# Optimization experiments

Measured on AMD Instinct MI355X. Metric: run time of the kernel, lower is better.

Reference implementation:

```python
import jax, jax.numpy as jnp
import numpy as np
from jax import lax

K = 3      # kernel_size
C = 64     # n_feat
B, H, W = 2, 256, 256


def _conv(x, w, b, pad):
    # NCHW conv, stride 1
    out = lax.conv_general_dilated(x, w, (1, 1), [(pad, pad), (pad, pad)],
                                   dimension_numbers=('NCHW', 'OIHW', 'NCHW'))
    return out + b[None, :, None, None]


def _prelu(x, a):
    # nn.PReLU() with a single shared learnable slope (init 0.25)
    return jnp.where(x >= 0, x, a * x)


def setup_inputs():
    key = jax.random.key(0)
    ks = jax.random.split(key, 20)
    s = 0.05
    def w(k, shape):
        return jax.random.normal(k, shape, jnp.float32) * s
    inp = {
        'image': jax.random.normal(ks[0], (B, C, H, W), jnp.float32),
        'guidance': jax.random.normal(ks[1], (B, C, H, W), jnp.float32),
        # self.tensor: 1x1 conv (2C -> C) + PReLU (shared with jbf_conv's act)
        'tensor_w': w(ks[2], (C, 2 * C, 1, 1)),
        'tensor_b': jnp.zeros((C,), jnp.float32),
        'a_jbf': jnp.full((1,), 0.25, jnp.float32),
        'kg_w1': w(ks[3], (C, C, 3, 3)), 'kg_b1': jnp.zeros((C,), jnp.float32),
        'kg_w2': w(ks[4], (C, C, 3, 3)), 'kg_b2': jnp.zeros((C,), jnp.float32),
        'kg_w3': w(ks[5], (C, C, 3, 3)), 'kg_b3': jnp.zeros((C,), jnp.float32),
        'kg_w4': w(ks[6], (C, C, 3, 3)), 'kg_b4': jnp.zeros((C,), jnp.float32),
        'kg_w5': w(ks[7], (K * K * C, C, 1, 1)),
        'kg_b5': jnp.zeros((K * K * C,), jnp.float32),
        'a_kg': jnp.full((1,), 0.25, jnp.float32),
        # jbf_conv: 3x3 C->C, PReLU (shared a_jbf), 3x3 C->C
        'jbf_w1': w(ks[8], (C, C, 3, 3)), 'jbf_b1': jnp.zeros((C,), jnp.float32),
        'jbf_w2': w(ks[9], (C, C, 3, 3)), 'jbf_b2': jnp.zeros((C,), jnp.float32),
    }
    return inp


def reference(image, guidance, tensor_w, tensor_b, a_jbf,
              kg_w1, kg_b1, kg_w2, kg_b2, kg_w3, kg_b3, kg_w4, kg_b4,
              kg_w5, kg_b5, a_kg, jbf_w1, jbf_b1, jbf_w2, jbf_b2):
    b, c, h, w = image.shape
    # fuse target+guidance features
    t = _prelu(_conv(jnp.concatenate([image, guidance], axis=1), tensor_w, tensor_b, 0), a_jbf)
    # concat_kg: predict per-pixel dynamic kernel (b, K*K*c, h, w)
    y = t
    for wt, bs in ((kg_w1, kg_b1), (kg_w2, kg_b2), (kg_w3, kg_b3), (kg_w4, kg_b4)):
        y = _prelu(_conv(y, wt, bs, 1), a_kg)
    bi_kernel = _conv(y, kg_w5, kg_b5, 0)
    # unfold: torch layout is channel-major (c, ki, kj) along dim 1
    p = (K - 1) // 2
    xp = jnp.pad(image, ((0, 0), (0, 0), (p, p), (p, p)))
    taps = [xp[:, :, i:i + h, j:j + w] for i in range(K) for j in range(K)]
    patch = jnp.stack(taps, axis=2).reshape(b, c * K * K, h, w)
    # NOTE: faithful to source -- (c*K*K) flat layout reinterpreted as (K*K, c)
    jbf = (patch * bi_kernel).reshape(b, K * K, c, h, w).sum(axis=1)
    out = _conv(_prelu(_conv(jbf, jbf_w1, jbf_b1, 1), a_jbf), jbf_w2, jbf_b2, 1)
    return out + image
```

## Files before the change

### kernel.cpp

```cpp
#include <hip/hip_runtime.h>

#define HW 65536

typedef __bf16 bf16x8 __attribute__((ext_vector_type(8)));
typedef float f32x16 __attribute__((ext_vector_type(16)));

__device__ inline unsigned short f2bf(float x) {
    union { float f; unsigned u; } v; v.f = x;
    unsigned r = v.u + 0x7FFF + ((v.u >> 16) & 1);
    return (unsigned short)(r >> 16);
}
__device__ inline float bfhi2f(unsigned u) {
    union { unsigned u; float f; } v; v.u = u & 0xffff0000u; return v.f;
}
__device__ inline float bflo2f(unsigned u) {
    union { unsigned u; float f; } v; v.u = u << 16; return v.f;
}

union FragU { uint4 u; bf16x8 v; };
__device__ inline bf16x8 ld_frag(const uint4* p) { FragU t; t.u = *p; return t.v; }

__global__ __launch_bounds__(256) void k_wprep(
    const float* __restrict__ w0, const float* __restrict__ w1,
    const float* __restrict__ w2, const float* __restrict__ w3,
    const float* __restrict__ w4, const float* __restrict__ w5,
    const float* __restrict__ w5c, const float* __restrict__ tw,
    unsigned short* __restrict__ wT)
{
    int y = blockIdx.y;
    unsigned short* o = wT + (size_t)y * 36864;
    if (y < 6) {
        const float* ws_[6] = {w0, w1, w2, w3, w4, w5};
        const float* w = ws_[y];
        for (int e = blockIdx.x * 256 + threadIdx.x; e < 36864; e += gridDim.x * 256) {
            int tap = e >> 12, oc = (e >> 6) & 63, ic = e & 63;
            int igg = ic >> 3, j = ic & 7;
            int dst = ((tap * 8 + igg) * 64 + oc) * 8 + j;
            o[dst] = f2bf(w[(oc * 64 + ic) * 9 + tap]);
        }
    } else if (y == 6) {
        for (int e = blockIdx.x * 256 + threadIdx.x; e < 36864; e += gridDim.x * 256)
            o[e] = f2bf(w5c[e]);
    } else {
        for (int e = blockIdx.x * 256 + threadIdx.x; e < 8192; e += gridDim.x * 256) {
            int oc = e >> 7, ic = e & 127;
            int kg = ic >> 3, j = ic & 7;
            o[((kg * 64 + oc) << 3) + j] = f2bf(tw[e]);
        }
    }
}

__global__ __launch_bounds__(256) void k_tr(
    const float* __restrict__ img, const float* __restrict__ gd,
    unsigned short* __restrict__ imgT, unsigned short* __restrict__ gdT)
{
    __shared__ float sT[64 * 66];
    int tid = threadIdx.x;
    int z = blockIdx.y;
    int b = z & 1;
    const float* src = (z >> 1) ? gd : img;
    unsigned short* dst = (z >> 1) ? gdT : imgT;
    int px0 = blockIdx.x * 64;
    size_t sbase = (size_t)b * 64 * HW + px0;

#pragma unroll
    for (int i = 0; i < 4; ++i) {
        int e = i * 256 + tid;
        int ic = e >> 4, seg = e & 15;
        float4 v = *(const float4*)(src + sbase + (size_t)ic * HW + seg * 4);
        float* p = &sT[ic * 66 + seg * 4];
        ((float2*)p)[0] = make_float2(v.x, v.y);
        ((float2*)p)[1] = make_float2(v.z, v.w);
    }
    __syncthreads();

    size_t dbase = (size_t)b * HW * 64 + (size_t)px0 * 64;
#pragma unroll
    for (int k = 0; k < 2; ++k) {
        int idx = k * 256 + tid;
        int px = idx >> 3, u = idx & 7;
        union { uint4 q; unsigned short h[8]; } o;
#pragma unroll
        for (int j = 0; j < 8; ++j)
            o.h[j] = f2bf(sT[(u * 8 + j) * 66 + px]);
        *(uint4*)(dst + dbase + (size_t)px * 64 + u * 8) = o.q;
    }
}

__global__ __launch_bounds__(256, 4) void k_fusem(
    const unsigned short* __restrict__ imgT, const unsigned short* __restrict__ gdT,
    const unsigned short* __restrict__ wTf, const float* __restrict__ bias,
    const float* __restrict__ a, unsigned short* __restrict__ out)
{
    __shared__ __align__(16) char smem[18688];
    uint4* sX = (uint4*)smem;
    float* sB = (float*)(smem + 18432);
    unsigned short* sT16 = (unsigned short*)smem;

    int tid = threadIdx.x;
    int wv = tid >> 6, lane = tid & 63;
    int half = lane >> 5, l31 = lane & 31;
    int b = blockIdx.z;
    int y0 = blockIdx.y * 8, x0 = blockIdx.x * 16;
    size_t zbase = (size_t)b * HW * 64;
    const uint4* wg = (const uint4*)wTf;

    if (tid < 64) sB[tid] = bias[tid];

    f32x16 acc[2];
#pragma unroll
    for (int i = 0; i < 2; ++i)
#pragma unroll
        for (int r = 0; r < 16; ++r) acc[i][r] = 0.f;

    auto loadX = [&](const unsigned short* src, uint4* rx) {
#pragma unroll
        for (int i = 0; i < 4; ++i) {
            int e = i * 256 + tid;
            int px = e >> 3, ig = e & 7;
            int gy = y0 + (px >> 4), gx = x0 + (px & 15);
            rx[i] = *(const uint4*)(src + zbase + ((size_t)(gy * 256 + gx)) * 64 + ig * 8);
        }
    };
    auto writeX = [&](const uint4* rx) {
#pragma unroll
        for (int i = 0; i < 4; ++i) {
            int e = i * 256 + tid;
            sX[(e >> 3) * 9 + (e & 7)] = rx[i];
        }
    };
    auto compute = [&](int h) {
#pragma unroll
        for (int c = 0; c < 4; ++c) {
            int ig = c * 2 + half;
            int kg = h * 8 + ig;
            bf16x8 a0 = ld_frag(&wg[kg * 64 + l31]);
            bf16x8 a1 = ld_frag(&wg[kg * 64 + 32 + l31]);
            int p0 = wv * 32 + l31;
            bf16x8 b0 = ld_frag(&sX[p0 * 9 + ig]);
            acc[0] = __builtin_amdgcn_mfma_f32_32x32x16_bf16(a0, b0, acc[0], 0, 0, 0);
            acc[1] = __builtin_amdgcn_mfma_f32_32x32x16_bf16(a1, b0, acc[1], 0, 0, 0);
        }
    };

    uint4 rx[4], ry[4];
    loadX(imgT, rx);
    writeX(rx);
    loadX(gdT, ry);
    __syncthreads();
    compute(0);
    __syncthreads();
    writeX(ry);
    __syncthreads();
    compute(1);

    float slope = a[0];
    __syncthreads();
    {
        int px = wv * 32 + l31;
#pragma unroll
        for (int ot = 0; ot < 2; ++ot)
#pragma unroll
            for (int q2 = 0; q2 < 4; ++q2) {
                unsigned short hw[4];
#pragma unroll
                for (int j = 0; j < 4; ++j) {
                    int r = (q2 << 2) | j;
                    int oc = ot * 32 + j + 8 * q2 + 4 * half;
                    float v = acc[ot][r] + sB[oc];
                    v = (v >= 0.f) ? v : slope * v;
                    hw[j] = f2bf(v);
                }
                int unit = ot * 4 + q2;
                int up = unit ^ (px & 7);
                uint2* p = (uint2*)&sT16[px * 64 + up * 8 + half * 4];
                *p = make_uint2((unsigned)hw[0] | ((unsigned)hw[1] << 16),
                                (unsigned)hw[2] | ((unsigned)hw[3] << 16));
            }
    }
    __syncthreads();
#pragma unroll
    for (int k = 0; k < 4; ++k) {
        int idx = k * 256 + tid;
        int row = idx >> 7, rem = idx & 127;
        int col = rem >> 3, u = rem & 7;
        int px = row * 16 + col;
        uint4 v = *(uint4*)&sT16[px * 64 + (u ^ (px & 7)) * 8];
        *(uint4*)(out + zbase + ((size_t)((y0 + row) * 256 + x0 + col)) * 64 + u * 8) = v;
    }
}

#define XU 5

template<int MODE>
__global__ __launch_bounds__(256, 4) void k_conv2x(
    const unsigned short* __restrict__ in,
    const unsigned short* __restrict__ w1T, const unsigned short* __restrict__ w2T,
    const float* __restrict__ b1, const float* __restrict__ b2,
    const float* __restrict__ a, const float* __restrict__ res,
    void* __restrict__ outv)
{
    __shared__ __align__(16) char smem[38912];
    uint4* sIn0 = (uint4*)smem;
    uint4* sIn1 = (uint4*)(smem + 19200);
    float* sB = (float*)(smem + 38400);

    int tid = threadIdx.x;
    int wv = tid >> 6, lane = tid & 63;
    int half = lane >> 5, l31 = lane & 31;
    int w2 = wv >> 1, g = wv & 1;
    int b = blockIdx.z;
    int y0 = blockIdx.y * 8, x0 = blockIdx.x * 16;
    const size_t zbase = (size_t)b * HW * 64;
    const uint4* wg1 = (const uint4*)w1T;
    const uint4* wg2 = (const uint4*)w2T;

    if (tid < 64) sB[tid] = b1[tid];
    else if (tid < 128) sB[tid] = b2[tid - 64];

    auto loadIn = [&](int h, uint4* rx) {
#pragma unroll
        for (int i = 0; i < 4; ++i) {
            int e = i * 256 + tid;
            int cell = e >> 2, ig = e & 3;
            int r = cell / 20, c2 = cell - r * 20;
            int gy = y0 - 2 + r, gx = x0 - 2 + c2;
            rx[i] = make_uint4(0, 0, 0, 0);
            bool act = (i < 3) || (e < 960);
            if (act && gy >= 0 && gy < 256 && gx >= 0 && gx < 256)
                rx[i] = *(const uint4*)(in + zbase + ((size_t)(gy * 256 + gx)) * 64 + h * 32 + ig * 8);
        }
    };
    auto writeIn = [&](uint4* s, const uint4* rx) {
#pragma unroll
        for (int i = 0; i < 4; ++i) {
            int e = i * 256 + tid;
            if (i < 3 || e < 960) s[(e >> 2) * XU + (e & 3)] = rx[i];
        }
    };

    int cellv[3], ibv[3];
#pragma unroll
    for (int s = 0; s < 3; ++s) {
        int c = g * 96 + s * 32 + l31;
        cellv[s] = c;
        int cc = c < 180 ? c : 179;
        ibv[s] = (cc / 18) * 20 + (cc % 18);
    }

    f32x16 acc1[3];
#pragma unroll
    for (int s = 0; s < 3; ++s)
#pragma unroll
        for (int r = 0; r < 16; ++r) acc1[s][r] = 0.f;

    auto conv1_h = [&](int h, const uint4* sInp) {
#pragma unroll
        for (int dy = 0; dy < 3; ++dy) {
#pragma unroll
            for (int dx = 0; dx < 3; ++dx) {
                int tap = dy * 3 + dx;
                int doff = dy * 20 + dx;
#pragma unroll
                for (int c = 0; c < 2; ++c) {
                    int ig = c * 2 + half;
                    bf16x8 af = ld_frag(&wg1[(tap * 8 + h * 4 + ig) * 64 + w2 * 32 + l31]);
#pragma unroll
                    for (int s = 0; s < 3; ++s) {
                        bf16x8 bb = ld_frag(&sInp[(ibv[s] + doff) * XU + ig]);
                        acc1[s] = __builtin_amdgcn_mfma_f32_32x32x16_bf16(af, bb, acc1[s], 0, 0, 0);
                    }
                }
            }
        }
    };

    uint4 rx[4];
    loadIn(0, rx);
    writeIn(sIn0, rx);
    uint4 ry[4];
    loadIn(1, ry);
    __syncthreads();
    conv1_h(0, sIn0);
    writeIn(sIn1, ry);
    __syncthreads();
    conv1_h(1, sIn1);

    float s1 = a[0];
    __syncthreads();
    unsigned short* sC16 = (unsigned short*)smem;
#pragma unroll
    for (int s = 0; s < 3; ++s) {
        int cell = cellv[s];
        if (cell < 180) {
            int orow = cell / 18, ocol = cell - orow * 18;
            int gy = y0 - 1 + orow, gx = x0 - 1 + ocol;
            bool inb = (gy >= 0 && gy < 256 && gx >= 0 && gx < 256);
#pragma unroll
            for (int q2 = 0; q2 < 4; ++q2) {
                unsigned short hw[4];
#pragma unroll
                for (int j = 0; j < 4; ++j) {
                    int r = (q2 << 2) | j;
                    int oc = w2 * 32 + j + 8 * q2 + 4 * half;
                    float v = acc1[s][r] + sB[oc];
                    v = (v >= 0.f) ? v : s1 * v;
                    if (!inb) v = 0.f;
                    hw[j] = f2bf(v);
                }
                int up = (w2 * 4 + q2) ^ (cell & 7);
                *(uint2*)&sC16[cell * 64 + up * 8 + half * 4] =
                    make_uint2((unsigned)hw[0] | ((unsigned)hw[1] << 16),
                               (unsigned)hw[2] | ((unsigned)hw[3] << 16));
            }
        }
    }
    __syncthreads();

    f32x16 acc2[2];
#pragma unroll
    for (int s = 0; s < 2; ++s)
#pragma unroll
        for (int r = 0; r < 16; ++r) acc2[s][r] = 0.f;

    int rowS[2], colS[2];
#pragma unroll
    for (int s = 0; s < 2; ++s) {
        int px = g * 64 + s * 32 + l31;
        rowS[s] = px >> 4; colS[s] = px & 15;
    }
    {
        const uint4* sC4 = (const uint4*)smem;
#pragma unroll
        for (int dy = 0; dy < 3; ++dy) {
#pragma unroll
            for (int dx = 0; dx < 3; ++dx) {
                int tap = dy * 3 + dx;
#pragma unroll
                for (int c = 0; c < 4; ++c) {
                    int ig = c * 2 + half;
                    bf16x8 af = ld_frag(&wg2[(tap * 8 + ig) * 64 + w2 * 32 + l31]);
#pragma unroll
                    for (int s = 0; s < 2; ++s) {
                        int cl = (rowS[s] + dy) * 18 + colS[s] + dx;
                        bf16x8 bb = ld_frag(&sC4[cl * 8 + (ig ^ (cl & 7))]);
                        acc2[s] = __builtin_amdgcn_mfma_f32_32x32x16_bf16(af, bb, acc2[s], 0, 0, 0);
                    }
                }
            }
        }
    }

    if (MODE == 0) {
        __syncthreads();
        unsigned short* sT16 = (unsigned short*)smem;
#pragma unroll
        for (int s = 0; s < 2; ++s) {
            int px = g * 64 + s * 32 + l31;
#pragma unroll
            for (int q2 = 0; q2 < 4; ++q2) {
                unsigned short hw[4];
#pragma unroll
                for (int j = 0; j < 4; ++j) {
                    int r = (q2 << 2) | j;
                    int oc = w2 * 32 + j + 8 * q2 + 4 * half;
                    float v = acc2[s][r] + sB[64 + oc];
                    v = (v >= 0.f) ? v : s1 * v;
                    hw[j] = f2bf(v);
                }
                int up = (w2 * 4 + q2) ^ (px & 7);
                uint2* p = (uint2*)&sT16[px * 64 + up * 8 + half * 4];
                *p = make_uint2((unsigned)hw[0] | ((unsigned)hw[1] << 16),
                                (unsigned)hw[2] | ((unsigned)hw[3] << 16));
            }
        }
        __syncthreads();
        unsigned short* outT = (unsigned short*)outv;
#pragma unroll
        for (int k = 0; k < 4; ++k) {
            int idx = k * 256 + tid;
            int row = idx >> 7, rem = idx & 127;
            int col = rem >> 3, u = rem & 7;
            int px = row * 16 + col;
            uint4 v = *(uint4*)&sT16[px * 64 + (u ^ (px & 7)) * 8];
            *(uint4*)(outT + zbase + ((size_t)((y0 + row) * 256 + x0 + col)) * 64 + u * 8) = v;
        }
    } else {
        float* outF = (float*)outv;
#pragma unroll
        for (int s = 0; s < 2; ++s) {
            int px = g * 64 + s * 32 + l31;
            int y = y0 + (px >> 4), x = x0 + (px & 15);
            size_t pbase = (size_t)b * 64 * HW + (size_t)y * 256 + x;
#pragma unroll
            for (int r = 0; r < 16; ++r) {
                int oc = w2 * 32 + (r & 3) + 8 * (r >> 2) + 4 * half;
                float v = acc2[s][r] + sB[64 + oc];
                v += res[pbase + (size_t)oc * HW];
                outF[pbase + (size_t)oc * HW] = v;
            }
        }
    }
}

struct OffTab { unsigned v[9][32]; int chlo[9]; };
constexpr OffTab make_tab() {
    OffTab t{};
    for (int kk = 0; kk < 9; ++kk) {
        int chlo = (kk * 64) / 9;
        t.chlo[kk] = chlo;
        for (int ot = 0; ot < 2; ++ot)
            for (int r = 0; r < 16; ++r) {
                int cc0 = ot * 32 + (r & 3) + 8 * (r >> 2);
                int q0 = kk * 64 + cc0, q1 = q0 + 4;
                int o0 = (q0 / 9 - chlo) * 360 + (q0 % 9 / 3) * 40 + (q0 % 9 % 3);
                int o1 = (q1 / 9 - chlo) * 360 + (q1 % 9 / 3) * 40 + (q1 % 9 % 3);
                t.v[kk][ot * 16 + r] = (unsigned)o0 | ((unsigned)o1 << 16);
            }
    }
    return t;
}
__constant__ OffTab kOff = make_tab();

__global__ __launch_bounds__(256, 2) void k_jbfm(
    const unsigned short* __restrict__ y4, const float* __restrict__ img,
    const unsigned short* __restrict__ w5T, const float* __restrict__ b5,
    unsigned short* __restrict__ out)
{
    __shared__ __align__(16) char smem[78592];
    uint4* sY = (uint4*)smem;
    float* sB5 = (float*)(smem + 76288);
    unsigned short* sT16 = (unsigned short*)smem;

    int tid = threadIdx.x;
    int wv = tid >> 6, lane = tid & 63;
    int half = lane >> 5, l31 = lane & 31;
    int b = blockIdx.z;
    int y0 = blockIdx.y * 8, x0 = blockIdx.x * 32;
    size_t zbase = (size_t)b * HW * 64;
    size_t ibase = (size_t)b * 64 * HW;

    int p_off[3], p_dst[3];
    bool p_a[3], p_b[3], p_act[3];
#pragma unroll
    for (int i = 0; i < 3; ++i) {
        int e = i * 256 + tid;
        bool act = e < 720;
        int ch = e / 90, rem = e - ch * 90;
        int rp = rem / 10, seg = rem - rp * 10;
        int gy = y0 + rp - 1;
        int gxb = x0 - 4 + seg * 4;
        bool xok = (gxb >= 0 && gxb < 256);
        p_act[i] = act;
        p_a[i] = act && xok && gy >= 0 && gy < 256;
        p_b[i] = act && xok && (gy + 1) < 256;
        p_off[i] = ch * HW + gy * 256 + gxb;
        p_dst[i] = ch * 360 + rp * 40 + seg * 4;
    }

#pragma unroll
    for (int i = 0; i < 8; ++i) {
        int e = i * 256 + tid;
        int px = e >> 3, ig = e & 7;
        int gy = y0 + (px >> 5), gx = x0 + (px & 31);
        sY[px * 9 + ig] = *(const uint4*)(y4 + zbase + ((size_t)(gy * 256 + gx)) * 64 + ig * 8);
    }
    for (int e = tid; e < 576; e += 256) sB5[e] = b5[e];

    {
        uint4* sW50 = (uint4*)(smem + 36864);
        unsigned* sP0 = (unsigned*)(smem + 53248);
#pragma unroll
        for (int u = 0; u < 2; ++u) {
            int uu = u * 256 + tid;
            int cc = uu & 63, ig = uu >> 6;
            sW50[uu] = ((const uint4*)w5T)[cc * 8 + ig];
        }
        const float* rp0 = img + ibase;
#pragma unroll
        for (int i = 0; i < 3; ++i) {
            float4 fa = make_float4(0, 0, 0, 0), fb = make_float4(0, 0, 0, 0);
            if (p_a[i]) fa = *(const float4*)(rp0 + p_off[i]);
            if (p_b[i]) fb = *(const float4*)(rp0 + p_off[i] + 256);
            if (p_act[i]) {
                uint4 pk;
                pk.x = (unsigned)f2bf(fa.x) | ((unsigned)f2bf(fb.x) << 16);
                pk.y = (unsigned)f2bf(fa.y) | ((unsigned)f2bf(fb.y) << 16);
                pk.z = (unsigned)f2bf(fa.z) | ((unsigned)f2bf(fb.z) << 16);
                pk.w = (unsigned)f2bf(fa.w) | ((unsigned)f2bf(fb.w) << 16);
                *(uint4*)&sP0[p_dst[i]] = pk;
            }
        }
    }

    float jb[2][2][16];
#pragma unroll
    for (int i = 0; i < 2; ++i)
#pragma unroll
        for (int j = 0; j < 2; ++j)
#pragma unroll
            for (int r = 0; r < 16; ++r) jb[i][j][r] = 0.f;

    __syncthreads();

#pragma unroll 1
    for (int kk = 0; kk < 9; ++kk) {
        const int cur = kk & 1;
        const uint4* sW5c = (const uint4*)(smem + 36864 + cur * 8192);
        const unsigned* sPc = (const unsigned*)(smem + 53248 + cur * 11520);

        uint4 wpre0, wpre1;
        float4 pfa[3], pfb[3];
        if (kk < 8) {
            const int nk = kk + 1;
            const int chlo_n = kOff.chlo[nk];
            {
                int cc = tid & 63, ig = tid >> 6;
                wpre0 = ((const uint4*)w5T)[(nk * 64 + cc) * 8 + ig];
                int uu = 256 + tid;
                int cc1 = uu & 63, ig1 = uu >> 6;
                wpre1 = ((const uint4*)w5T)[(nk * 64 + cc1) * 8 + ig1];
            }
            const float* rp0 = img + ibase + (size_t)chlo_n * HW;
#pragma unroll
            for (int i = 0; i < 3; ++i) {
                pfa[i] = make_float4(0, 0, 0, 0);
                pfb[i] = make_float4(0, 0, 0, 0);
                if (p_a[i]) pfa[i] = *(const float4*)(rp0 + p_off[i]);
                if (p_b[i]) pfb[i] = *(const float4*)(rp0 + p_off[i] + 256);
            }
        }

        f32x16 acc[2][2];
#pragma unroll
        for (int ot = 0; ot < 2; ++ot)
#pragma unroll
            for (int r = 0; r < 16; ++r) {
                int cc0 = ot * 32 + (r & 3) + 8 * (r >> 2);
                float bv = sB5[kk * 64 + cc0 + 4 * half];
                acc[ot][0][r] = bv;
                acc[ot][1][r] = bv;
            }

#pragma unroll
        for (int c = 0; c < 4; ++c) {
            int ig = c * 2 + half;
            bf16x8 a0 = ld_frag(&sW5c[ig * 64 + l31]);
            bf16x8 a1 = ld_frag(&sW5c[ig * 64 + 32 + l31]);
            int p0 = wv * 64 + l31;
            bf16x8 b0 = ld_frag(&sY[p0 * 9 + ig]);
            bf16x8 b1 = ld_frag(&sY[(p0 + 32) * 9 + ig]);
            acc[0][0] = __builtin_amdgcn_mfma_f32_32x32x16_bf16(a0, b0, acc[0][0], 0, 0, 0);
            acc[0][1] = __builtin_amdgcn_mfma_f32_32x32x16_bf16(a0, b1, acc[0][1], 0, 0, 0);
            acc[1][0] = __builtin_amdgcn_mfma_f32_32x32x16_bf16(a1, b0, acc[1][0], 0, 0, 0);
            acc[1][1] = __builtin_amdgcn_mfma_f32_32x32x16_bf16(a1, b1, acc[1][1], 0, 0, 0);
        }

        {
            const unsigned* basep = sPc + wv * 80 + l31 + 3;
            const unsigned* tab = kOff.v[kk];
#pragma unroll
            for (int ot = 0; ot < 2; ++ot)
#pragma unroll
                for (int r = 0; r < 16; ++r) {
                    unsigned oo = tab[ot * 16 + r];
                    unsigned o0 = oo & 0xffffu, o1 = oo >> 16;
                    unsigned pv = basep[half ? o1 : o0];
                    jb[ot][0][r] = fmaf(acc[ot][0][r], bflo2f(pv), jb[ot][0][r]);
                    jb[ot][1][r] = fmaf(acc[ot][1][r], bfhi2f(pv), jb[ot][1][r]);
                }
        }

        if (kk < 8) {
            uint4* sW5n = (uint4*)(smem + 36864 + (cur ^ 1) * 8192);
            unsigned* sPn = (unsigned*)(smem + 53248 + (cur ^ 1) * 11520);
            sW5n[tid] = wpre0;
            sW5n[256 + tid] = wpre1;
#pragma unroll
            for (int i = 0; i < 3; ++i) {
                if (p_act[i]) {
                    uint4 pk;
                    pk.x = (unsigned)f2bf(pfa[i].x) | ((unsigned)f2bf(pfb[i].x) << 16);
                    pk.y = (unsigned)f2bf(pfa[i].y) | ((unsigned)f2bf(pfb[i].y) << 16);
                    pk.z = (unsigned)f2bf(pfa[i].z) | ((unsigned)f2bf(pfb[i].z) << 16);
                    pk.w = (unsigned)f2bf(pfa[i].w) | ((unsigned)f2bf(pfb[i].w) << 16);
                    *(uint4*)&sPn[p_dst[i]] = pk;
                }
            }
        }
        __syncthreads();
    }

#pragma unroll
    for (int ot = 0; ot < 2; ++ot)
#pragma unroll
        for (int pt = 0; pt < 2; ++pt) {
            int px = wv * 64 + pt * 32 + l31;
#pragma unroll
            for (int q2 = 0; q2 < 4; ++q2) {
                unsigned short hw[4];
#pragma unroll
                for (int j = 0; j < 4; ++j) {
                    int r = (q2 << 2) | j;
                    hw[j] = f2bf(jb[ot][pt][r]);
                }
                int unit = ot * 4 + q2;
                int up = unit ^ (px & 7);
                uint2* p = (uint2*)&sT16[px * 64 + up * 8 + half * 4];
                *p = make_uint2((unsigned)hw[0] | ((unsigned)hw[1] << 16),
                                (unsigned)hw[2] | ((unsigned)hw[3] << 16));
            }
        }
    __syncthreads();
#pragma unroll
    for (int k = 0; k < 8; ++k) {
        int col = tid >> 3, u = tid & 7;
        int px = k * 32 + col;
        uint4 v = *(uint4*)&sT16[px * 64 + (u ^ (px & 7)) * 8];
        *(uint4*)(out + zbase + ((size_t)((y0 + k) * 256 + x0 + col)) * 64 + u * 8) = v;
    }
}

extern "C" void kernel_launch(void* const* d_in, const int* in_sizes, int n_in,
                              void* d_out, int out_size, void* d_ws, size_t ws_size,
                              hipStream_t stream) {
    const float* img  = (const float*)d_in[0];
    const float* gd   = (const float*)d_in[1];
    const float* tw   = (const float*)d_in[2];
    const float* tb   = (const float*)d_in[3];
    const float* ajbf = (const float*)d_in[4];
    const float* kw1  = (const float*)d_in[5];
    const float* kb1  = (const float*)d_in[6];
    const float* kw2  = (const float*)d_in[7];
    const float* kb2  = (const float*)d_in[8];
    const float* kw3  = (const float*)d_in[9];
    const float* kb3  = (const float*)d_in[10];
    const float* kw4  = (const float*)d_in[11];
    const float* kb4  = (const float*)d_in[12];
    const float* kw5  = (const float*)d_in[13];
    const float* kb5  = (const float*)d_in[14];
    const float* akg  = (const float*)d_in[15];
    const float* jw1  = (const float*)d_in[16];
    const float* jb1  = (const float*)d_in[17];
    const float* jw2  = (const float*)d_in[18];
    const float* jb2  = (const float*)d_in[19];
    float* out  = (float*)d_out;

    const size_t TEN = (size_t)2 * HW * 64;
    unsigned short* bufA = (unsigned short*)d_ws;
    unsigned short* imgT = bufA + TEN;
    unsigned short* gdT  = imgT + TEN;
    unsigned short* wT   = gdT + TEN;
    unsigned short* bufB = (unsigned short*)d_out;
    unsigned short* bufC = gdT;

    dim3 gs(16, 32, 2);
    dim3 gw(8, 32, 2);

    k_tr<<<dim3(1024, 4), 256, 0, stream>>>(img, gd, imgT, gdT);
    k_wprep<<<dim3(4, 8), 256, 0, stream>>>(kw1, kw2, kw3, kw4, jw1, jw2, kw5, tw, wT);

    k_fusem<<<gs, 256, 0, stream>>>(imgT, gdT, wT + (size_t)7 * 36864, tb, ajbf, bufA);

    k_conv2x<0><<<gs, 256, 0, stream>>>(bufA, wT + (size_t)0 * 36864, wT + (size_t)1 * 36864,
                                        kb1, kb2, akg, nullptr, bufB);
    k_conv2x<0><<<gs, 256, 0, stream>>>(bufB, wT + (size_t)2 * 36864, wT + (size_t)3 * 36864,
                                        kb3, kb4, akg, nullptr, bufA);

    k_jbfm<<<gw, 256, 0, stream>>>(bufA, img, wT + (size_t)6 * 36864, kb5, bufC);

    k_conv2x<2><<<gs, 256, 0, stream>>>(bufC, wT + (size_t)4 * 36864, wT + (size_t)5 * 36864,
                                        jb1, jb2, ajbf, img, out);
}
```

Baseline: 311.5 us.

## Fuse conv stages into one persistent cooperative kernel with grid barriers

Replaces the five separate stage launches (fuse, two double-conv, jbf, final double-conv) with one persistent 512-block kernel. The blocks loop over tiles and synchronise between stages with a software grid barrier built on an atomic counter that k_wprep resets. This removes launch gaps and per-kernel tail effects. In exchange, every block uses the largest shared-memory footprint (78 KB) at occupancy 2, so the conv stages lose occupancy, and each stage boundary adds barrier spin cost.

Result: slower. 762.6 us (+144.8%).

```diff
diff --git a/kernel.cpp b/kernel.cpp
--- a/kernel.cpp
+++ b/kernel.cpp
@@ -25,10 +25,11 @@
     const float* __restrict__ w2, const float* __restrict__ w3,
     const float* __restrict__ w4, const float* __restrict__ w5,
     const float* __restrict__ w5c, const float* __restrict__ tw,
-    unsigned short* __restrict__ wT)
+    unsigned short* __restrict__ wT, unsigned long long* __restrict__ bar)
 {
     int y = blockIdx.y;
     unsigned short* o = wT + (size_t)y * 36864;
+    if (y == 7 && blockIdx.x == 0 && threadIdx.x == 0) *bar = 0ull;
     if (y < 6) {
         const float* ws_[6] = {w0, w1, w2, w3, w4, w5};
         const float* w = ws_[y];
@@ -87,24 +88,41 @@
     }
 }
 
-__global__ __launch_bounds__(256, 4) void k_fusem(
-    const unsigned short* __restrict__ imgT, const unsigned short* __restrict__ gdT,
-    const unsigned short* __restrict__ wTf, const float* __restrict__ bias,
-    const float* __restrict__ a, unsigned short* __restrict__ out)
+__device__ __forceinline__ void gbar(unsigned long long* bar, bool wb) {
+    __syncthreads();
+    if (threadIdx.x == 0) {
+        if (wb) __builtin_amdgcn_fence(__ATOMIC_RELEASE, "agent");
+        unsigned long long v = __hip_atomic_fetch_add(bar, 1ull,
+            __ATOMIC_RELAXED, __HIP_MEMORY_SCOPE_AGENT);
+        unsigned g = (unsigned)(v >> 32);
+        unsigned c = (unsigned)v;
+        if (c == 511u) {
+            __hip_atomic_store(bar, (unsigned long long)(g + 1u) << 32,
+                __ATOMIC_RELAXED, __HIP_MEMORY_SCOPE_AGENT);
+        } else {
+            while ((unsigned)(__hip_atomic_load(bar, __ATOMIC_RELAXED,
+                       __HIP_MEMORY_SCOPE_AGENT) >> 32) == g)
+                __builtin_amdgcn_s_sleep(8);
+        }
+    }
+    __syncthreads();
+}
+
+__device__ __forceinline__ void st_fusem(char* smem, int tid, int t,
+    const unsigned short* imgT, const unsigned short* gdT, const uint4* wg,
+    const float* bias, const float* a, unsigned short* out)
 {
-    __shared__ __align__(16) char smem[18688];
     uint4* sX = (uint4*)smem;
     float* sB = (float*)(smem + 18432);
     unsigned short* sT16 = (unsigned short*)smem;
 
-    int tid = threadIdx.x;
     int wv = tid >> 6, lane = tid & 63;
     int half = lane >> 5, l31 = lane & 31;
-    int b = blockIdx.z;
-    int y0 = blockIdx.y * 8, x0 = blockIdx.x * 16;
+    int b = t >> 9, rem = t & 511;
+    int y0 = (rem >> 4) * 8, x0 = (rem & 15) * 16;
     size_t zbase = (size_t)b * HW * 64;
-    const uint4* wg = (const uint4*)wTf;
-
+
+    __syncthreads();
     if (tid < 64) sB[tid] = bias[tid];
 
     f32x16 acc[2];
@@ -171,8 +189,7 @@
                     v = (v >= 0.f) ? v : slope * v;
                     hw[j] = f2bf(v);
                 }
-                int unit = ot * 4 + q2;
-                int up = unit ^ (px & 7);
+                int up = (ot * 4 + q2) ^ (px & 7);
                 uint2* p = (uint2*)&sT16[px * 64 + up * 8 + half * 4];
                 *p = make_uint2((unsigned)hw[0] | ((unsigned)hw[1] << 16),
                                 (unsigned)hw[2] | ((unsigned)hw[3] << 16));
@@ -182,8 +199,8 @@
 #pragma unroll
     for (int k = 0; k < 4; ++k) {
         int idx = k * 256 + tid;
-        int row = idx >> 7, rem = idx & 127;
-        int col = rem >> 3, u = rem & 7;
+        int row = idx >> 7, rem2 = idx & 127;
+        int col = rem2 >> 3, u = rem2 & 7;
         int px = row * 16 + col;
         uint4 v = *(uint4*)&sT16[px * 64 + (u ^ (px & 7)) * 8];
         *(uint4*)(out + zbase + ((size_t)((y0 + row) * 256 + x0 + col)) * 64 + u * 8) = v;
@@ -193,28 +210,23 @@
 #define XU 5
 
 template<int MODE>
-__global__ __launch_bounds__(256, 4) void k_conv2x(
-    const unsigned short* __restrict__ in,
-    const unsigned short* __restrict__ w1T, const unsigned short* __restrict__ w2T,
-    const float* __restrict__ b1, const float* __restrict__ b2,
-    const float* __restrict__ a, const float* __restrict__ res,
-    void* __restrict__ outv)
+__device__ __forceinline__ void st_conv2x(char* smem, int tid, int t,
+    const unsigned short* in, const uint4* wg1, const uint4* wg2,
+    const float* b1, const float* b2, const float* a,
+    const float* res, void* outv)
 {
-    __shared__ __align__(16) char smem[38912];
     uint4* sIn0 = (uint4*)smem;
     uint4* sIn1 = (uint4*)(smem + 19200);
     float* sB = (float*)(smem + 38400);
 
-    int tid = threadIdx.x;
     int wv = tid >> 6, lane = tid & 63;
     int half = lane >> 5, l31 = lane & 31;
     int w2 = wv >> 1, g = wv & 1;
-    int b = blockIdx.z;
-    int y0 = blockIdx.y * 8, x0 = blockIdx.x * 16;
+    int b = t >> 9, rem = t & 511;
+    int y0 = (rem >> 4) * 8, x0 = (rem & 15) * 16;
     const size_t zbase = (size_t)b * HW * 64;
-    const uint4* wg1 = (const uint4*)w1T;
-    const uint4* wg2 = (const uint4*)w2T;
-
+
+    __syncthreads();
     if (tid < 64) sB[tid] = b1[tid];
     else if (tid < 128) sB[tid] = b2[tid - 64];
 
@@ -379,8 +391,8 @@
 #pragma unroll
         for (int k = 0; k < 4; ++k) {
             int idx = k * 256 + tid;
-            int row = idx >> 7, rem = idx & 127;
-            int col = rem >> 3, u = rem & 7;
+            int row = idx >> 7, rem2 = idx & 127;
+            int col = rem2 >> 3, u = rem2 & 7;
             int px = row * 16 + col;
             uint4 v = *(uint4*)&sT16[px * 64 + (u ^ (px & 7)) * 8];
             *(uint4*)(outT + zbase + ((size_t)((y0 + row) * 256 + x0 + col)) * 64 + u * 8) = v;
@@ -422,23 +434,22 @@
 }
 __constant__ OffTab kOff = make_tab();
 
-__global__ __launch_bounds__(256, 2) void k_jbfm(
-    const unsigned short* __restrict__ y4, const float* __restrict__ img,
-    const unsigned short* __restrict__ w5T, const float* __restrict__ b5,
-    unsigned short* __restrict__ out)
+__device__ __forceinline__ void st_jbfm(char* smem, int tid, int t,
+    const unsigned short* y4, const float* img,
+    const unsigned short* w5T, const float* b5, unsigned short* out)
 {
-    __shared__ __align__(16) char smem[78592];
     uint4* sY = (uint4*)smem;
     float* sB5 = (float*)(smem + 76288);
     unsigned short* sT16 = (unsigned short*)smem;
 
-    int tid = threadIdx.x;
     int wv = tid >> 6, lane = tid & 63;
     int half = lane >> 5, l31 = lane & 31;
-    int b = blockIdx.z;
-    int y0 = blockIdx.y * 8, x0 = blockIdx.x * 32;
+    int b = t >> 8, rem = t & 255;
+    int y0 = (rem >> 3) * 8, x0 = (rem & 7) * 32;
     size_t zbase = (size_t)b * HW * 64;
     size_t ibase = (size_t)b * 64 * HW;
+
+    __syncthreads();
 
     int p_off[3], p_dst[3];
     bool p_a[3], p_b[3], p_act[3];
@@ -446,8 +457,8 @@
     for (int i = 0; i < 3; ++i) {
         int e = i * 256 + tid;
         bool act = e < 720;
-        int ch = e / 90, rem = e - ch * 90;
-        int rp = rem / 10, seg = rem - rp * 10;
+        int ch = e / 90, rem2 = e - ch * 90;
+        int rp = rem2 / 10, seg = rem2 - rp * 10;
         int gy = y0 + rp - 1;
         int gxb = x0 - 4 + seg * 4;
         bool xok = (gxb >= 0 && gxb < 256);
@@ -604,8 +615,7 @@
                     int r = (q2 << 2) | j;
                     hw[j] = f2bf(jb[ot][pt][r]);
                 }
-                int unit = ot * 4 + q2;
-                int up = unit ^ (px & 7);
+                int up = (ot * 4 + q2) ^ (px & 7);
                 uint2* p = (uint2*)&sT16[px * 64 + up * 8 + half * 4];
                 *p = make_uint2((unsigned)hw[0] | ((unsigned)hw[1] << 16),
                                 (unsigned)hw[2] | ((unsigned)hw[3] << 16));
@@ -619,6 +629,51 @@
         uint4 v = *(uint4*)&sT16[px * 64 + (u ^ (px & 7)) * 8];
         *(uint4*)(out + zbase + ((size_t)((y0 + k) * 256 + x0 + col)) * 64 + u * 8) = v;
     }
+}
+
+__global__ __launch_bounds__(256, 2) void k_mega(
+    unsigned short* imgT, unsigned short* gdT, const unsigned short* wT,
+    const float* tb, const float* ajbf, const float* akg,
+    const float* kb1, const float* kb2, const float* kb3, const float* kb4,
+    const float* kb5, const float* jb1, const float* jb2,
+    const float* img, unsigned short* bufA, void* dout,
+    unsigned long long* bar)
+{
+    __shared__ __align__(16) char smem[78592];
+    int tid = threadIdx.x;
+    int bid = blockIdx.x;
+    int slab = bid & 7, sub = bid >> 3;
+
+#pragma unroll 1
+    for (int j = 0; j < 2; ++j)
+        st_fusem(smem, tid, slab * 128 + j * 64 + sub, imgT, gdT,
+                 (const uint4*)(wT + (size_t)7 * 36864), tb, ajbf, bufA);
+    gbar(bar, true);
+
+#pragma unroll 1
+    for (int j = 0; j < 2; ++j)
+        st_conv2x<0>(smem, tid, slab * 128 + j * 64 + sub, bufA,
+                     (const uint4*)wT, (const uint4*)(wT + (size_t)1 * 36864),
+                     kb1, kb2, akg, nullptr, dout);
+    gbar(bar, true);
+
+#pragma unroll 1
+    for (int j = 0; j < 2; ++j)
+        st_conv2x<0>(smem, tid, slab * 128 + j * 64 + sub,
+                     (const unsigned short*)dout,
+                     (const uint4*)(wT + (size_t)2 * 36864), (const uint4*)(wT + (size_t)3 * 36864),
+                     kb3, kb4, akg, nullptr, imgT);
+    gbar(bar, false);
+
+    st_jbfm(smem, tid, slab * 64 + sub, imgT, img,
+            wT + (size_t)6 * 36864, kb5, gdT);
+    gbar(bar, true);
+
+#pragma unroll 1
+    for (int j = 0; j < 2; ++j)
+        st_conv2x<2>(smem, tid, slab * 128 + j * 64 + sub, gdT,
+                     (const uint4*)(wT + (size_t)4 * 36864), (const uint4*)(wT + (size_t)5 * 36864),
+                     jb1, jb2, ajbf, img, dout);
 }
 
 extern "C" void kernel_launch(void* const* d_in, const int* in_sizes, int n_in,
@@ -644,31 +699,31 @@
     const float* jb1  = (const float*)d_in[17];
     const float* jw2  = (const float*)d_in[18];
     const float* jb2  = (const float*)d_in[19];
-    float* out  = (float*)d_out;
 
     const size_t TEN = (size_t)2 * HW * 64;
     unsigned short* bufA = (unsigned short*)d_ws;
     unsigned short* imgT = bufA + TEN;
     unsigned short* gdT  = imgT + TEN;
     unsigned short* wT   = gdT + TEN;
-    unsigned short* bufB = (unsigned short*)d_out;
-    unsigned short* bufC = gdT;
-
-    dim3 gs(16, 32, 2);
-    dim3 gw(8, 32, 2);
+    unsigned long long* bar = (unsigned long long*)(wT + (size_t)8 * 36864);
+    void* doutv = d_out;
 
     k_tr<<<dim3(1024, 4), 256, 0, stream>>>(img, gd, imgT, gdT);
-    k_wprep<<<dim3(4, 8), 256, 0, stream>>>(kw1, kw2, kw3, kw4, jw1, jw2, kw5, tw, wT);
-
-    k_fusem<<<gs, 256, 0, stream>>>(imgT, gdT, wT + (size_t)7 * 36864, tb, ajbf, bufA);
-
-    k_conv2x<0><<<gs, 256, 0, stream>>>(bufA, wT + (size_t)0 * 36864, wT + (size_t)1 * 36864,
-                                        kb1, kb2, akg, nullptr, bufB);
-    k_conv2x<0><<<gs, 256, 0, stream>>>(bufB, wT + (size_t)2 * 36864, wT + (size_t)3 * 36864,
-                                        kb3, kb4, akg, nullptr, bufA);
-
-    k_jbfm<<<gw, 256, 0, stream>>>(bufA, img, wT + (size_t)6 * 36864, kb5, bufC);
-
-    k_conv2x<2><<<gs, 256, 0, stream>>>(bufC, wT + (size_t)4 * 36864, wT + (size_t)5 * 36864,
-                                        jb1, jb2, ajbf, img, out);
-}
+    k_wprep<<<dim3(4, 8), 256, 0, stream>>>(kw1, kw2, kw3, kw4, jw1, jw2, kw5, tw, wT, bar);
+
+    const unsigned short* wTc = wT;
+    const float* imgc = img;
+    void* kargs[] = {
+        (void*)&imgT, (void*)&gdT, (void*)&wTc,
+        (void*)&tb, (void*)&ajbf, (void*)&akg,
+        (void*)&kb1, (void*)&kb2, (void*)&kb3, (void*)&kb4,
+        (void*)&kb5, (void*)&jb1, (void*)&jb2,
+        (void*)&imgc, (void*)&bufA, (void*)&doutv, (void*)&bar
+    };
+    if (hipLaunchCooperativeKernel((void*)k_mega, dim3(512), dim3(256),
+                                   kargs, 0, stream) != hipSuccess) {
+        k_mega<<<dim3(512), dim3(256), 0, stream>>>(
+            imgT, gdT, wTc, tb, ajbf, akg, kb1, kb2, kb3, kb4,
+            kb5, jb1, jb2, imgc, bufA, doutv, bar);
+    }
+}
```
